# Optimization experiments

Hardware: AMD Instinct MI355X
Metric: run time of the kernel (lower is better)

## Reference

```python
import jax, jax.numpy as jnp
import numpy as np
from jax import lax

K = 31      # avg_pool kernel
PAD = 15    # padding (count_include_pad=True -> divide by K*K always)
LAMBDA1 = 1.0
LAMBDA2 = 1.0


def _box_mean(x):
    # 31x31 stride-1 avg pool with zero padding, divisor = K*K (torch default count_include_pad=True)
    s = lax.reduce_window(x, 0.0, lax.add, (1, 1, K, K), (1, 1, 1, 1),
                          [(0, 0), (0, 0), (PAD, PAD), (PAD, PAD)])
    return s / float(K * K)


def setup_inputs() -> dict:
    key = jax.random.key(0)
    k1, k2 = jax.random.split(key)
    pred = jax.random.normal(k1, (64, 1, 512, 512), dtype=jnp.float32)
    mask = jax.random.uniform(k2, (64, 1, 512, 512), dtype=jnp.float32)
    return {"pred": pred, "mask": mask}


def reference(pred, mask):
    weit = 1.0 + 5.0 * jnp.abs(_box_mean(mask) - mask)
    # bce_with_logits, numerically stable: max(x,0) - x*y + log1p(exp(-|x|))
    bce = jnp.maximum(pred, 0.0) - pred * mask + jnp.log1p(jnp.exp(-jnp.abs(pred)))
    # NOTE: original torch code passes reduce='none' (deprecated kwarg, truthy string),
    # which resolves to reduction='mean' -> wbce is a SCALAR; the (weit*.)/weit.sum
    # normalization then cancels exactly. We reproduce that behavior faithfully.
    wbce = jnp.mean(bce)  # scalar, broadcast over (B, C)
    p = jax.nn.sigmoid(pred)
    inter = jnp.sum(p * mask * weit, axis=(2, 3))       # [B, C]
    union = jnp.sum((p + mask) * weit, axis=(2, 3))     # [B, C]
    wiou = 1.0 - (inter + 1.0) / (union - inter + 1.0)  # [B, C]
    return jnp.mean(LAMBDA1 * wbce + LAMBDA2 * wiou)
```

## Files before the change

kernel.cpp:

```cpp
#include <hip/hip_runtime.h>
#include <math.h>

#define BATCH 64
#define HH 512
#define WW 512
#define PAD 15
#define NELEM ((size_t)BATCH * HH * WW)
#define INV_KK (1.0f / 961.0f)

#define TILE_H 16
#define BPI (HH / TILE_H)
#define NBLK (BATCH * BPI)
#define NXCD 8

typedef float f4 __attribute__((ext_vector_type(4)));

__device__ __forceinline__ float wave_reduce(float v) {
    #pragma unroll
    for (int off = 32; off; off >>= 1) v += __shfl_down(v, off, 64);
    return v;
}

__global__ __launch_bounds__(256) void fused_kernel(const float* __restrict__ pred,
                                                    const float* __restrict__ mask,
                                                    double* __restrict__ partials) {
    __shared__ float vrow[4][WW];
    __shared__ float P[4][WW];
    __shared__ float red[3][4];

    const int f    = blockIdx.x;
    const int xcd  = f & (NXCD - 1);
    const int slot = f >> 3;
    const int img  = xcd * 8 + (slot >> 5);
    const int tile = slot & (BPI - 1);

    const int tid  = threadIdx.x;
    const int lane = tid & 63;
    const int wv   = tid >> 6;
    const int h0   = tile * TILE_H;
    const int c0   = tid;
    const int c1   = tid + 256;

    const float* mb = mask + (size_t)img * HH * WW;
    const float* pb = pred + (size_t)img * HH * WW;

    float r0 = 0.0f, r1 = 0.0f;
    {
        int lo = h0 - PAD; if (lo < 0) lo = 0;
        int hi = h0 + PAD; if (hi > HH - 1) hi = HH - 1;
        for (int y = lo; y <= hi; ++y) {
            r0 += mb[(size_t)y * WW + c0];
            r1 += mb[(size_t)y * WW + c1];
        }
    }

    float accb = 0.0f, acci = 0.0f, accu = 0.0f;

    #pragma unroll 1
    for (int it = 0; it < TILE_H / 4; ++it) {
        const int hbase = h0 + it * 4;

        #pragma unroll
        for (int j = 0; j < 4; ++j) {
            const int h = hbase + j;
            vrow[j][c0] = r0;
            vrow[j][c1] = r1;
            const int add = h + PAD + 1;
            const int sub = h - PAD;
            float a0 = 0.0f, a1 = 0.0f, s0 = 0.0f, s1 = 0.0f;
            if (add < HH) { a0 = mb[(size_t)add * WW + c0]; a1 = mb[(size_t)add * WW + c1]; }
            if (sub >= 0) { s0 = mb[(size_t)sub * WW + c0]; s1 = mb[(size_t)sub * WW + c1]; }
            r0 += a0 - s0;
            r1 += a1 - s1;
        }
        __syncthreads();

        const int h = hbase + wv;
        const size_t rbase = (size_t)h * WW;

        f4 va = *(const f4*)&vrow[wv][8 * lane];
        f4 vb = *(const f4*)&vrow[wv][8 * lane + 4];
        float p0 = va.x;
        float p1 = p0 + va.y;
        float p2 = p1 + va.z;
        float p3 = p2 + va.w;
        float p4 = p3 + vb.x;
        float p5 = p4 + vb.y;
        float p6 = p5 + vb.z;
        float p7 = p6 + vb.w;
        float lanesum = p7;
        float incl = lanesum;
        #pragma unroll
        for (int off = 1; off < 64; off <<= 1) {
            float n = __shfl_up(incl, off, 64);
            if (lane >= off) incl += n;
        }
        const float excl = incl - lanesum;
        f4 Pa, Pb;
        Pa.x = excl + p0; Pa.y = excl + p1; Pa.z = excl + p2; Pa.w = excl + p3;
        Pb.x = excl + p4; Pb.y = excl + p5; Pb.z = excl + p6; Pb.w = excl + p7;
        *(f4*)&P[wv][8 * lane]     = Pa;
        *(f4*)&P[wv][8 * lane + 4] = Pb;

        #pragma unroll
        for (int k = 0; k < 8; ++k) {
            const int w = lane + 64 * k;
            int hiw = w + PAD; if (hiw > WW - 1) hiw = WW - 1;
            float s = P[wv][hiw];
            if (w >= PAD + 1) s -= P[wv][w - PAD - 1];

            const float m  = mb[rbase + w];
            const float pr = pb[rbase + w];

            const float weit = 1.0f + 5.0f * fabsf(s * INV_KK - m);
            const float e    = __expf(-fabsf(pr));
            const float bce  = fmaxf(pr, 0.0f) - pr * m + __logf(1.0f + e);
            const float inv  = __builtin_amdgcn_rcpf(1.0f + e);
            const float p    = (pr >= 0.0f) ? inv : e * inv;

            accb += bce;
            acci += p * m * weit;
            accu += (p + m) * weit;
        }
        __syncthreads();
    }

    accb = wave_reduce(accb);
    acci = wave_reduce(acci);
    accu = wave_reduce(accu);
    if (lane == 0) { red[0][wv] = accb; red[1][wv] = acci; red[2][wv] = accu; }
    __syncthreads();
    if (tid == 0) {
        double bt = (double)red[0][0] + red[0][1] + red[0][2] + red[0][3];
        double it2 = (double)red[1][0] + red[1][1] + red[1][2] + red[1][3];
        double ut = (double)red[2][0] + red[2][1] + red[2][2] + red[2][3];
        const size_t pidx = (size_t)img * BPI + tile;
        partials[pidx * 3 + 0] = bt;
        partials[pidx * 3 + 1] = it2;
        partials[pidx * 3 + 2] = ut;
    }
}

__global__ __launch_bounds__(256) void finalize_kernel(const double* __restrict__ partials,
                                                       float* __restrict__ out) {
    __shared__ double redbce[4];
    int tid = threadIdx.x, lane = tid & 63, wv = tid >> 6;

    double bsum = 0.0;
    for (int i = tid; i < NBLK; i += 256) bsum += partials[(size_t)i * 3 + 0];
    #pragma unroll
    for (int off = 32; off; off >>= 1) bsum += __shfl_down(bsum, off, 64);
    if (lane == 0) redbce[wv] = bsum;
    __syncthreads();

    double wiou_term = 0.0;
    if (tid < 64) {
        int bb = tid;
        double it = 0.0, ut = 0.0;
        for (int j = 0; j < BPI; ++j) {
            it += partials[(size_t)(bb * BPI + j) * 3 + 1];
            ut += partials[(size_t)(bb * BPI + j) * 3 + 2];
        }
        wiou_term = 1.0 - (it + 1.0) / (ut - it + 1.0);
    }
    if (wv == 0) {
        #pragma unroll
        for (int off = 32; off; off >>= 1) wiou_term += __shfl_down(wiou_term, off, 64);
    }
    if (tid == 0) {
        double wbce = (redbce[0] + redbce[1] + redbce[2] + redbce[3]) / (double)NELEM;
        out[0] = (float)(wbce + wiou_term * (1.0 / 64.0));
    }
}

#define ACC_DOUBLES 129
__global__ __launch_bounds__(256) void rowpass_nows_kernel(const float* __restrict__ pred,
                                                           const float* __restrict__ mask,
                                                           double* __restrict__ acc) {
    __shared__ float vrow1[WW];
    __shared__ float red[3][4];
    int b = blockIdx.x / HH;
    int h = blockIdx.x % HH;
    int lo = h - PAD; if (lo < 0) lo = 0;
    int hi = h + PAD; if (hi > HH - 1) hi = HH - 1;
    float s0 = 0.0f, s1 = 0.0f;
    const float* mb = mask + (size_t)b * HH * WW;
    for (int y = lo; y <= hi; ++y) {
        s0 += mb[(size_t)y * WW + threadIdx.x];
        s1 += mb[(size_t)y * WW + threadIdx.x + 256];
    }
    vrow1[threadIdx.x]       = s0;
    vrow1[threadIdx.x + 256] = s1;
    __syncthreads();

    size_t base = ((size_t)b * HH + h) * WW;
    float bce_p = 0.0f, inter_p = 0.0f, uni_p = 0.0f;
    for (int w = threadIdx.x; w < WW; w += 256) {
        int wlo = w - PAD; if (wlo < 0) wlo = 0;
        int whi = w + PAD; if (whi > WW - 1) whi = WW - 1;
        float s = 0.0f;
        for (int k = wlo; k <= whi; ++k) s += vrow1[k];
        float m  = mask[base + w];
        float pr = pred[base + w];
        float weit = 1.0f + 5.0f * fabsf(s * INV_KK - m);
        float e   = expf(-fabsf(pr));
        float bce = fmaxf(pr, 0.0f) - pr * m + log1pf(e);
        float inv = 1.0f / (1.0f + e);
        float p   = (pr >= 0.0f) ? inv : e * inv;
        bce_p += bce; inter_p += p * m * weit; uni_p += (p + m) * weit;
    }
    int lane = threadIdx.x & 63, wvv = threadIdx.x >> 6;
    bce_p = wave_reduce(bce_p); inter_p = wave_reduce(inter_p); uni_p = wave_reduce(uni_p);
    if (lane == 0) { red[0][wvv] = bce_p; red[1][wvv] = inter_p; red[2][wvv] = uni_p; }
    __syncthreads();
    if (threadIdx.x == 0) {
        atomicAdd(&acc[0], (double)(red[0][0] + red[0][1] + red[0][2] + red[0][3]));
        atomicAdd(&acc[1 + b], (double)(red[1][0] + red[1][1] + red[1][2] + red[1][3]));
        atomicAdd(&acc[65 + b], (double)(red[2][0] + red[2][1] + red[2][2] + red[2][3]));
    }
}

__global__ void finalize_atomic_kernel(const double* __restrict__ acc, float* __restrict__ out) {
    int b = threadIdx.x;
    double inter = acc[1 + b];
    double uni   = acc[65 + b];
    double wiou = 1.0 - (inter + 1.0) / (uni - inter + 1.0);
    #pragma unroll
    for (int off = 32; off; off >>= 1) wiou += __shfl_down(wiou, off, 64);
    if (b == 0) {
        double wbce = acc[0] / (double)NELEM;
        out[0] = (float)(wbce + wiou * (1.0 / 64.0));
    }
}

extern "C" void kernel_launch(void* const* d_in, const int* in_sizes, int n_in,
                              void* d_out, int out_size, void* d_ws, size_t ws_size,
                              hipStream_t stream) {
    const float* pred = (const float*)d_in[0];
    const float* mask = (const float*)d_in[1];
    float* out = (float*)d_out;

    const size_t part_bytes = (size_t)NBLK * 3 * sizeof(double);

    if (ws_size >= part_bytes) {
        double* partials = (double*)d_ws;
        fused_kernel<<<NBLK, 256, 0, stream>>>(pred, mask, partials);
        finalize_kernel<<<1, 256, 0, stream>>>(partials, out);
    } else {
        double* acc = (double*)d_ws;
        hipMemsetAsync(acc, 0, ACC_DOUBLES * sizeof(double), stream);
        rowpass_nows_kernel<<<BATCH * HH, 256, 0, stream>>>(pred, mask, acc);
        finalize_atomic_kernel<<<1, 64, 0, stream>>>(acc, out);
    }
}
```

Measured before the change: 61.63 us.

## Double tile height, prefetch next sliding-window rows, double-buffer column sums

```diff
diff --git a/kernel.cpp b/kernel.cpp
--- a/kernel.cpp
+++ b/kernel.cpp
@@ -8,7 +8,8 @@
 #define NELEM ((size_t)BATCH * HH * WW)
 #define INV_KK (1.0f / 961.0f)
 
-#define TILE_H 16
+#define TILE_H 32
+#define NIT (TILE_H / 4)
 #define BPI (HH / TILE_H)
 #define NBLK (BATCH * BPI)
 #define NXCD 8
@@ -24,14 +25,14 @@
 __global__ __launch_bounds__(256) void fused_kernel(const float* __restrict__ pred,
                                                     const float* __restrict__ mask,
                                                     double* __restrict__ partials) {
-    __shared__ float vrow[4][WW];
+    __shared__ float vrow[2][4][WW];
     __shared__ float P[4][WW];
     __shared__ float red[3][4];
 
     const int f    = blockIdx.x;
     const int xcd  = f & (NXCD - 1);
     const int slot = f >> 3;
-    const int img  = xcd * 8 + (slot >> 5);
+    const int img  = xcd * 8 + (slot >> 4);
     const int tile = slot & (BPI - 1);
 
     const int tid  = threadIdx.x;
@@ -54,40 +55,62 @@
         }
     }
 
+    float pa0, pa1, pa2, pa3, ps0, ps1, ps2, ps3;
+    float qa0, qa1, qa2, qa3, qs0, qs1, qs2, qs3;
+
+    #define PREFETCH(ii)                                                       \
+    {                                                                          \
+        const int hb = h0 + 4 * (ii);                                          \
+        const int a0r = hb + 16, a1r = hb + 17, a2r = hb + 18, a3r = hb + 19;  \
+        const int s0r = hb - 15, s1r = hb - 14, s2r = hb - 13, s3r = hb - 12;  \
+        pa0 = (a0r < HH) ? mb[(size_t)a0r * WW + c0] : 0.0f;                   \
+        pa1 = (a1r < HH) ? mb[(size_t)a1r * WW + c0] : 0.0f;                   \
+        pa2 = (a2r < HH) ? mb[(size_t)a2r * WW + c0] : 0.0f;                   \
+        pa3 = (a3r < HH) ? mb[(size_t)a3r * WW + c0] : 0.0f;                   \
+        ps0 = (s0r >= 0) ? mb[(size_t)s0r * WW + c0] : 0.0f;                   \
+        ps1 = (s1r >= 0) ? mb[(size_t)s1r * WW + c0] : 0.0f;                   \
+        ps2 = (s2r >= 0) ? mb[(size_t)s2r * WW + c0] : 0.0f;                   \
+        ps3 = (s3r >= 0) ? mb[(size_t)s3r * WW + c0] : 0.0f;                   \
+        qa0 = (a0r < HH) ? mb[(size_t)a0r * WW + c1] : 0.0f;                   \
+        qa1 = (a1r < HH) ? mb[(size_t)a1r * WW + c1] : 0.0f;                   \
+        qa2 = (a2r < HH) ? mb[(size_t)a2r * WW + c1] : 0.0f;                   \
+        qa3 = (a3r < HH) ? mb[(size_t)a3r * WW + c1] : 0.0f;                   \
+        qs0 = (s0r >= 0) ? mb[(size_t)s0r * WW + c1] : 0.0f;                   \
+        qs1 = (s1r >= 0) ? mb[(size_t)s1r * WW + c1] : 0.0f;                   \
+        qs2 = (s2r >= 0) ? mb[(size_t)s2r * WW + c1] : 0.0f;                   \
+        qs3 = (s3r >= 0) ? mb[(size_t)s3r * WW + c1] : 0.0f;                   \
+    }
+
+    PREFETCH(0)
+
     float accb = 0.0f, acci = 0.0f, accu = 0.0f;
 
     #pragma unroll 1
-    for (int it = 0; it < TILE_H / 4; ++it) {
+    for (int it = 0; it < NIT; ++it) {
         const int hbase = h0 + it * 4;
-
-        #pragma unroll
-        for (int j = 0; j < 4; ++j) {
-            const int h = hbase + j;
-            vrow[j][c0] = r0;
-            vrow[j][c1] = r1;
-            const int add = h + PAD + 1;
-            const int sub = h - PAD;
-            float a0 = 0.0f, a1 = 0.0f, s0 = 0.0f, s1 = 0.0f;
-            if (add < HH) { a0 = mb[(size_t)add * WW + c0]; a1 = mb[(size_t)add * WW + c1]; }
-            if (sub >= 0) { s0 = mb[(size_t)sub * WW + c0]; s1 = mb[(size_t)sub * WW + c1]; }
-            r0 += a0 - s0;
-            r1 += a1 - s1;
-        }
+        float (*vb)[WW] = vrow[it & 1];
+
+        vb[0][c0] = r0; vb[0][c1] = r1; r0 += pa0 - ps0; r1 += qa0 - qs0;
+        vb[1][c0] = r0; vb[1][c1] = r1; r0 += pa1 - ps1; r1 += qa1 - qs1;
+        vb[2][c0] = r0; vb[2][c1] = r1; r0 += pa2 - ps2; r1 += qa2 - qs2;
+        vb[3][c0] = r0; vb[3][c1] = r1; r0 += pa3 - ps3; r1 += qa3 - qs3;
         __syncthreads();
+
+        if (it + 1 < NIT) PREFETCH(it + 1)
 
         const int h = hbase + wv;
         const size_t rbase = (size_t)h * WW;
 
-        f4 va = *(const f4*)&vrow[wv][8 * lane];
-        f4 vb = *(const f4*)&vrow[wv][8 * lane + 4];
+        f4 va = *(const f4*)&vb[wv][8 * lane];
+        f4 vbv = *(const f4*)&vb[wv][8 * lane + 4];
         float p0 = va.x;
         float p1 = p0 + va.y;
         float p2 = p1 + va.z;
         float p3 = p2 + va.w;
-        float p4 = p3 + vb.x;
-        float p5 = p4 + vb.y;
-        float p6 = p5 + vb.z;
-        float p7 = p6 + vb.w;
+        float p4 = p3 + vbv.x;
+        float p5 = p4 + vbv.y;
+        float p6 = p5 + vbv.z;
+        float p7 = p6 + vbv.w;
         float lanesum = p7;
         float incl = lanesum;
         #pragma unroll
@@ -122,8 +145,8 @@
             acci += p * m * weit;
             accu += (p + m) * weit;
         }
-        __syncthreads();
-    }
+    }
+    #undef PREFETCH
 
     accb = wave_reduce(accb);
     acci = wave_reduce(acci);
```

Result: faster. 51.53 us (-16.4%).

## Double-buffer row sums, prefetch mask rows, and process two rows per wave

Applied to the files above, without the earlier changes.

```diff
diff --git a/kernel.cpp b/kernel.cpp
--- a/kernel.cpp
+++ b/kernel.cpp
@@ -8,7 +8,9 @@
 #define NELEM ((size_t)BATCH * HH * WW)
 #define INV_KK (1.0f / 961.0f)
 
-#define TILE_H 16
+#define TILE_H 32
+#define RPI 8
+#define NIT (TILE_H / RPI)
 #define BPI (HH / TILE_H)
 #define NBLK (BATCH * BPI)
 #define NXCD 8
@@ -24,14 +26,13 @@
 __global__ __launch_bounds__(256) void fused_kernel(const float* __restrict__ pred,
                                                     const float* __restrict__ mask,
                                                     double* __restrict__ partials) {
-    __shared__ float vrow[4][WW];
-    __shared__ float P[4][WW];
+    __shared__ float vrow[2][RPI][WW];
     __shared__ float red[3][4];
 
     const int f    = blockIdx.x;
     const int xcd  = f & (NXCD - 1);
     const int slot = f >> 3;
-    const int img  = xcd * 8 + (slot >> 5);
+    const int img  = xcd * 8 + (slot >> 4);
     const int tile = slot & (BPI - 1);
 
     const int tid  = threadIdx.x;
@@ -54,76 +55,124 @@
         }
     }
 
+    float pa[RPI], ps[RPI], qa[RPI], qs[RPI];
+
+    #define PREFETCH(ii)                                                   \
+    {                                                                      \
+        const int hb = h0 + RPI * (ii);                                    \
+        _Pragma("unroll")                                                  \
+        for (int j = 0; j < RPI; ++j) {                                    \
+            const int ar = hb + 16 + j;                                    \
+            const int sr = hb - 15 + j;                                    \
+            pa[j] = (ar < HH) ? mb[(size_t)ar * WW + c0] : 0.0f;           \
+            qa[j] = (ar < HH) ? mb[(size_t)ar * WW + c1] : 0.0f;           \
+            ps[j] = (sr >= 0) ? mb[(size_t)sr * WW + c0] : 0.0f;           \
+            qs[j] = (sr >= 0) ? mb[(size_t)sr * WW + c1] : 0.0f;           \
+        }                                                                  \
+    }
+
+    PREFETCH(0)
+
     float accb = 0.0f, acci = 0.0f, accu = 0.0f;
 
     #pragma unroll 1
-    for (int it = 0; it < TILE_H / 4; ++it) {
-        const int hbase = h0 + it * 4;
-
-        #pragma unroll
-        for (int j = 0; j < 4; ++j) {
-            const int h = hbase + j;
-            vrow[j][c0] = r0;
-            vrow[j][c1] = r1;
-            const int add = h + PAD + 1;
-            const int sub = h - PAD;
-            float a0 = 0.0f, a1 = 0.0f, s0 = 0.0f, s1 = 0.0f;
-            if (add < HH) { a0 = mb[(size_t)add * WW + c0]; a1 = mb[(size_t)add * WW + c1]; }
-            if (sub >= 0) { s0 = mb[(size_t)sub * WW + c0]; s1 = mb[(size_t)sub * WW + c1]; }
-            r0 += a0 - s0;
-            r1 += a1 - s1;
+    for (int it = 0; it < NIT; ++it) {
+        const int hbase = h0 + it * RPI;
+        float (*vb)[WW] = vrow[it & 1];
+
+        #pragma unroll
+        for (int j = 0; j < RPI; ++j) {
+            vb[j][c0] = r0;
+            vb[j][c1] = r1;
+            r0 += pa[j] - ps[j];
+            r1 += qa[j] - qs[j];
         }
         __syncthreads();
 
-        const int h = hbase + wv;
-        const size_t rbase = (size_t)h * WW;
-
-        f4 va = *(const f4*)&vrow[wv][8 * lane];
-        f4 vb = *(const f4*)&vrow[wv][8 * lane + 4];
-        float p0 = va.x;
-        float p1 = p0 + va.y;
-        float p2 = p1 + va.z;
-        float p3 = p2 + va.w;
-        float p4 = p3 + vb.x;
-        float p5 = p4 + vb.y;
-        float p6 = p5 + vb.z;
-        float p7 = p6 + vb.w;
-        float lanesum = p7;
-        float incl = lanesum;
+        if (it + 1 < NIT) PREFETCH(it + 1)
+
+        const int ra = 2 * wv;
+        const int rbr = ra + 1;
+        const int hA = hbase + ra;
+        const int hB = hA + 1;
+        const size_t rbA = (size_t)hA * WW;
+        const size_t rbB = (size_t)hB * WW;
+
+        float prA[8], prB[8];
+        #pragma unroll
+        for (int k = 0; k < 8; ++k) {
+            prA[k] = pb[rbA + lane + 64 * k];
+            prB[k] = pb[rbB + lane + 64 * k];
+        }
+
+        f4 a0 = *(const f4*)&vb[ra][8 * lane];
+        f4 a1 = *(const f4*)&vb[ra][8 * lane + 4];
+        f4 b0 = *(const f4*)&vb[rbr][8 * lane];
+        f4 b1 = *(const f4*)&vb[rbr][8 * lane + 4];
+        float A0 = a0.x,      B0 = b0.x;
+        float A1 = A0 + a0.y, B1 = B0 + b0.y;
+        float A2 = A1 + a0.z, B2 = B1 + b0.z;
+        float A3 = A2 + a0.w, B3 = B2 + b0.w;
+        float A4 = A3 + a1.x, B4 = B3 + b1.x;
+        float A5 = A4 + a1.y, B5 = B4 + b1.y;
+        float A6 = A5 + a1.z, B6 = B5 + b1.z;
+        float A7 = A6 + a1.w, B7 = B6 + b1.w;
+        float inclA = A7, inclB = B7;
         #pragma unroll
         for (int off = 1; off < 64; off <<= 1) {
-            float n = __shfl_up(incl, off, 64);
-            if (lane >= off) incl += n;
-        }
-        const float excl = incl - lanesum;
-        f4 Pa, Pb;
-        Pa.x = excl + p0; Pa.y = excl + p1; Pa.z = excl + p2; Pa.w = excl + p3;
-        Pb.x = excl + p4; Pb.y = excl + p5; Pb.z = excl + p6; Pb.w = excl + p7;
-        *(f4*)&P[wv][8 * lane]     = Pa;
-        *(f4*)&P[wv][8 * lane + 4] = Pb;
+            float nA = __shfl_up(inclA, off, 64);
+            float nB = __shfl_up(inclB, off, 64);
+            if (lane >= off) { inclA += nA; inclB += nB; }
+        }
+        const float exA = inclA - A7;
+        const float exB = inclB - B7;
+        f4 wa0, wa1, wb0, wb1;
+        wa0.x = exA + A0; wa0.y = exA + A1; wa0.z = exA + A2; wa0.w = exA + A3;
+        wa1.x = exA + A4; wa1.y = exA + A5; wa1.z = exA + A6; wa1.w = exA + A7;
+        wb0.x = exB + B0; wb0.y = exB + B1; wb0.z = exB + B2; wb0.w = exB + B3;
+        wb1.x = exB + B4; wb1.y = exB + B5; wb1.z = exB + B6; wb1.w = exB + B7;
+        *(f4*)&vb[ra][8 * lane]      = wa0;
+        *(f4*)&vb[ra][8 * lane + 4]  = wa1;
+        *(f4*)&vb[rbr][8 * lane]     = wb0;
+        *(f4*)&vb[rbr][8 * lane + 4] = wb1;
 
         #pragma unroll
         for (int k = 0; k < 8; ++k) {
             const int w = lane + 64 * k;
             int hiw = w + PAD; if (hiw > WW - 1) hiw = WW - 1;
-            float s = P[wv][hiw];
-            if (w >= PAD + 1) s -= P[wv][w - PAD - 1];
-
-            const float m  = mb[rbase + w];
-            const float pr = pb[rbase + w];
-
-            const float weit = 1.0f + 5.0f * fabsf(s * INV_KK - m);
-            const float e    = __expf(-fabsf(pr));
-            const float bce  = fmaxf(pr, 0.0f) - pr * m + __logf(1.0f + e);
-            const float inv  = __builtin_amdgcn_rcpf(1.0f + e);
-            const float p    = (pr >= 0.0f) ? inv : e * inv;
-
-            accb += bce;
-            acci += p * m * weit;
-            accu += (p + m) * weit;
-        }
-        __syncthreads();
-    }
+            const int low = w - PAD - 1;
+
+            float sA = vb[ra][hiw];
+            float sB = vb[rbr][hiw];
+            if (low >= 0) { sA -= vb[ra][low]; sB -= vb[rbr][low]; }
+
+            {
+                const float m  = mb[rbA + w];
+                const float pr = prA[k];
+                const float weit = 1.0f + 5.0f * fabsf(sA * INV_KK - m);
+                const float e    = __expf(-fabsf(pr));
+                const float bce  = fmaxf(pr, 0.0f) - pr * m + __logf(1.0f + e);
+                const float inv  = __builtin_amdgcn_rcpf(1.0f + e);
+                const float p    = (pr >= 0.0f) ? inv : e * inv;
+                accb += bce;
+                acci += p * m * weit;
+                accu += (p + m) * weit;
+            }
+            {
+                const float m  = mb[rbB + w];
+                const float pr = prB[k];
+                const float weit = 1.0f + 5.0f * fabsf(sB * INV_KK - m);
+                const float e    = __expf(-fabsf(pr));
+                const float bce  = fmaxf(pr, 0.0f) - pr * m + __logf(1.0f + e);
+                const float inv  = __builtin_amdgcn_rcpf(1.0f + e);
+                const float p    = (pr >= 0.0f) ? inv : e * inv;
+                accb += bce;
+                acci += p * m * weit;
+                accu += (p + m) * weit;
+            }
+        }
+    }
+    #undef PREFETCH
 
     accb = wave_reduce(accb);
     acci = wave_reduce(acci);
```

Result: faster. 53.76 us (-12.8%).

## Double-buffer column sums, prefetch mask rows, widen blocks to 512 threads

Applied to the files above, without the earlier changes.

```diff
diff --git a/kernel.cpp b/kernel.cpp
--- a/kernel.cpp
+++ b/kernel.cpp
@@ -8,7 +8,10 @@
 #define NELEM ((size_t)BATCH * HH * WW)
 #define INV_KK (1.0f / 961.0f)
 
-#define TILE_H 16
+#define THREADS 512
+#define TILE_H 32
+#define RPI 8
+#define NIT (TILE_H / RPI)
 #define BPI (HH / TILE_H)
 #define NBLK (BATCH * BPI)
 #define NXCD 8
@@ -21,73 +24,80 @@
     return v;
 }
 
-__global__ __launch_bounds__(256) void fused_kernel(const float* __restrict__ pred,
-                                                    const float* __restrict__ mask,
-                                                    double* __restrict__ partials) {
-    __shared__ float vrow[4][WW];
-    __shared__ float P[4][WW];
-    __shared__ float red[3][4];
+__global__ __launch_bounds__(THREADS) void fused_kernel(const float* __restrict__ pred,
+                                                        const float* __restrict__ mask,
+                                                        double* __restrict__ partials) {
+    __shared__ float vrow[2][RPI][WW];
+    __shared__ float red[3][8];
 
     const int f    = blockIdx.x;
     const int xcd  = f & (NXCD - 1);
     const int slot = f >> 3;
-    const int img  = xcd * 8 + (slot >> 5);
+    const int img  = xcd * 8 + (slot >> 4);
     const int tile = slot & (BPI - 1);
 
     const int tid  = threadIdx.x;
     const int lane = tid & 63;
     const int wv   = tid >> 6;
     const int h0   = tile * TILE_H;
-    const int c0   = tid;
-    const int c1   = tid + 256;
+    const int c    = tid;
 
     const float* mb = mask + (size_t)img * HH * WW;
     const float* pb = pred + (size_t)img * HH * WW;
 
-    float r0 = 0.0f, r1 = 0.0f;
+    float r = 0.0f;
     {
         int lo = h0 - PAD; if (lo < 0) lo = 0;
         int hi = h0 + PAD; if (hi > HH - 1) hi = HH - 1;
-        for (int y = lo; y <= hi; ++y) {
-            r0 += mb[(size_t)y * WW + c0];
-            r1 += mb[(size_t)y * WW + c1];
-        }
-    }
+        for (int y = lo; y <= hi; ++y) r += mb[(size_t)y * WW + c];
+    }
+
+    float pa[RPI], ps[RPI];
+
+    #define PREFETCH(ii)                                                   \
+    {                                                                      \
+        const int hb = h0 + RPI * (ii);                                    \
+        _Pragma("unroll")                                                  \
+        for (int j = 0; j < RPI; ++j) {                                    \
+            const int ar = hb + 16 + j;                                    \
+            const int sr = hb - 15 + j;                                    \
+            pa[j] = (ar < HH) ? mb[(size_t)ar * WW + c] : 0.0f;            \
+            ps[j] = (sr >= 0) ? mb[(size_t)sr * WW + c] : 0.0f;            \
+        }                                                                  \
+    }
+
+    PREFETCH(0)
 
     float accb = 0.0f, acci = 0.0f, accu = 0.0f;
 
     #pragma unroll 1
-    for (int it = 0; it < TILE_H / 4; ++it) {
-        const int hbase = h0 + it * 4;
-
-        #pragma unroll
-        for (int j = 0; j < 4; ++j) {
-            const int h = hbase + j;
-            vrow[j][c0] = r0;
-            vrow[j][c1] = r1;
-            const int add = h + PAD + 1;
-            const int sub = h - PAD;
-            float a0 = 0.0f, a1 = 0.0f, s0 = 0.0f, s1 = 0.0f;
-            if (add < HH) { a0 = mb[(size_t)add * WW + c0]; a1 = mb[(size_t)add * WW + c1]; }
-            if (sub >= 0) { s0 = mb[(size_t)sub * WW + c0]; s1 = mb[(size_t)sub * WW + c1]; }
-            r0 += a0 - s0;
-            r1 += a1 - s1;
+    for (int it = 0; it < NIT; ++it) {
+        const int hbase = h0 + it * RPI;
+        float (*vb)[WW] = vrow[it & 1];
+
+        #pragma unroll
+        for (int j = 0; j < RPI; ++j) {
+            vb[j][c] = r;
+            r += pa[j] - ps[j];
         }
         __syncthreads();
+
+        if (it + 1 < NIT) PREFETCH(it + 1)
 
         const int h = hbase + wv;
         const size_t rbase = (size_t)h * WW;
-
-        f4 va = *(const f4*)&vrow[wv][8 * lane];
-        f4 vb = *(const f4*)&vrow[wv][8 * lane + 4];
+        float* row = vb[wv];
+
+        f4 va = *(const f4*)&row[8 * lane];
+        f4 vc = *(const f4*)&row[8 * lane + 4];
         float p0 = va.x;
         float p1 = p0 + va.y;
         float p2 = p1 + va.z;
         float p3 = p2 + va.w;
-        float p4 = p3 + vb.x;
-        float p5 = p4 + vb.y;
-        float p6 = p5 + vb.z;
-        float p7 = p6 + vb.w;
+        float p4 = p3 + vc.x;
+        float p5 = p4 + vc.y;
+        float p6 = p5 + vc.z;
+        float p7 = p6 + vc.w;
         float lanesum = p7;
         float incl = lanesum;
         #pragma unroll
@@ -99,15 +109,15 @@
         f4 Pa, Pb;
         Pa.x = excl + p0; Pa.y = excl + p1; Pa.z = excl + p2; Pa.w = excl + p3;
         Pb.x = excl + p4; Pb.y = excl + p5; Pb.z = excl + p6; Pb.w = excl + p7;
-        *(f4*)&P[wv][8 * lane]     = Pa;
-        *(f4*)&P[wv][8 * lane + 4] = Pb;
+        *(f4*)&row[8 * lane]     = Pa;
+        *(f4*)&row[8 * lane + 4] = Pb;
 
         #pragma unroll
         for (int k = 0; k < 8; ++k) {
             const int w = lane + 64 * k;
             int hiw = w + PAD; if (hiw > WW - 1) hiw = WW - 1;
-            float s = P[wv][hiw];
-            if (w >= PAD + 1) s -= P[wv][w - PAD - 1];
+            float s = row[hiw];
+            if (w >= PAD + 1) s -= row[w - PAD - 1];
 
             const float m  = mb[rbase + w];
             const float pr = pb[rbase + w];
@@ -122,8 +132,8 @@
             acci += p * m * weit;
             accu += (p + m) * weit;
         }
-        __syncthreads();
-    }
+    }
+    #undef PREFETCH
 
     accb = wave_reduce(accb);
     acci = wave_reduce(acci);
@@ -131,9 +141,11 @@
     if (lane == 0) { red[0][wv] = accb; red[1][wv] = acci; red[2][wv] = accu; }
     __syncthreads();
     if (tid == 0) {
-        double bt = (double)red[0][0] + red[0][1] + red[0][2] + red[0][3];
-        double it2 = (double)red[1][0] + red[1][1] + red[1][2] + red[1][3];
-        double ut = (double)red[2][0] + red[2][1] + red[2][2] + red[2][3];
+        double bt = 0.0, it2 = 0.0, ut = 0.0;
+        #pragma unroll
+        for (int j = 0; j < 8; ++j) {
+            bt += red[0][j]; it2 += red[1][j]; ut += red[2][j];
+        }
         const size_t pidx = (size_t)img * BPI + tile;
         partials[pidx * 3 + 0] = bt;
         partials[pidx * 3 + 1] = it2;
@@ -244,7 +256,7 @@
 
     if (ws_size >= part_bytes) {
         double* partials = (double*)d_ws;
-        fused_kernel<<<NBLK, 256, 0, stream>>>(pred, mask, partials);
+        fused_kernel<<<NBLK, THREADS, 0, stream>>>(pred, mask, partials);
         finalize_kernel<<<1, 256, 0, stream>>>(partials, out);
     } else {
         double* acc = (double*)d_ws;
```

Result: slower. 65.09 us (+5.6%).
